# Kernel tuning notes

Hardware: AMD Instinct MI355X
Metric: run time of the kernel (lower is better)

Reference implementation:

```python
import jax, jax.numpy as jnp
import numpy as np

BATCH, FLAT_IN, PROJ_DIM, HEADS, ACT_DIM = 2048, 512, 256, 16384, 64


def setup_inputs() -> dict:
    key = jax.random.key(0)
    k1, k2, k3, k4 = jax.random.split(key, 4)
    state = jax.random.normal(k1, (BATCH, FLAT_IN), dtype=jnp.float32)
    random_projection = jax.random.normal(k2, (FLAT_IN, PROJ_DIM), dtype=jnp.float32)
    memories = jax.random.normal(k3, (HEADS, PROJ_DIM), dtype=jnp.float32)
    logits = jax.random.normal(k4, (HEADS, ACT_DIM), dtype=jnp.float32)
    return {"state": state, "random_projection": random_projection,
            "memories": memories, "logits": logits}


def reference(state, random_projection, memories, logits):
    # state: [B, flat_in] -> projected [B, proj_dim] (proj_dim branch of __call__)
    s = state.reshape(state.shape[0], -1) @ random_projection
    # sum(state[:,None] * memories[None,:], -1) == dot-product similarity GEMM
    similarities = jnp.einsum('bd,hd->bh', s, memories)  # [B, heads]
    closest = jnp.argmax(similarities, axis=1)           # [B]
    return logits[closest]                                # [B, act_dim]
```

## Files before the change

kernel.cpp:

```cpp
#include <hip/hip_runtime.h>

#define BATCH    2048
#define FLAT_IN  512
#define PROJ_DIM 256
#define HEADS    16384
#define ACT_DIM  64

typedef __attribute__((ext_vector_type(8))) short short8;
typedef _Float16 half8 __attribute__((ext_vector_type(8)));
typedef __attribute__((ext_vector_type(4))) float floatx4;

__device__ __forceinline__ unsigned short f2bf(float x) {
  unsigned u = __float_as_uint(x);
  u += 0x7fff + ((u >> 16) & 1);
  return (unsigned short)(u >> 16);
}
__device__ __forceinline__ float bf2f(unsigned short b) {
  return __uint_as_float(((unsigned)b) << 16);
}
__device__ __forceinline__ unsigned short f2h(float x) {
  _Float16 h = (_Float16)x;
  return __builtin_bit_cast(unsigned short, h);
}

#define GLDS16(g, l)                                                          \
  __builtin_amdgcn_global_load_lds(                                           \
      (__attribute__((address_space(1))) void*)(void*)(g),                    \
      (__attribute__((address_space(3))) void*)(l), 16, 0, 0)

__global__ __launch_bounds__(256) void prep(
    const float* __restrict__ state, const float* __restrict__ rp,
    unsigned short* __restrict__ st_hi, unsigned short* __restrict__ st_mid,
    unsigned short* __restrict__ rpT_hi, unsigned short* __restrict__ rpT_mid)
{
  const int tid = threadIdx.x;
  const int b = blockIdx.x;
  if (b < 1024) {
    int i = b * 256 + tid;
    float4 v = ((const float4*)state)[i];
    ushort4 h, m;
    h.x = f2bf(v.x); m.x = f2bf(v.x - bf2f(h.x));
    h.y = f2bf(v.y); m.y = f2bf(v.y - bf2f(h.y));
    h.z = f2bf(v.z); m.z = f2bf(v.z - bf2f(h.z));
    h.w = f2bf(v.w); m.w = f2bf(v.w - bf2f(h.w));
    ((ushort4*)st_hi)[i]  = h;
    ((ushort4*)st_mid)[i] = m;
  } else {
    __shared__ float t[64][65];
    int bid = b - 1024;
    int k0 = (bid >> 2) * 64, n0 = (bid & 3) * 64;
#pragma unroll
    for (int it = 0; it < 16; ++it) {
      int lin = it * 256 + tid;
      int kr = lin >> 6, nc = lin & 63;
      t[kr][nc] = rp[(size_t)(k0 + kr) * PROJ_DIM + n0 + nc];
    }
    __syncthreads();
#pragma unroll
    for (int it = 0; it < 16; ++it) {
      int lin = it * 256 + tid;
      int nr = lin >> 6, kc = lin & 63;
      float v = t[kc][nr];
      unsigned short hh = f2bf(v);
      rpT_hi [(size_t)(n0 + nr) * FLAT_IN + k0 + kc] = hh;
      rpT_mid[(size_t)(n0 + nr) * FLAT_IN + k0 + kc] = f2bf(v - bf2f(hh));
    }
  }
}

__global__ __launch_bounds__(256, 2) void gemm_conv(
    const unsigned short* __restrict__ Ahi, const unsigned short* __restrict__ Amid,
    const unsigned short* __restrict__ Bhi, const unsigned short* __restrict__ Bmid,
    const float* __restrict__ mem,
    float* __restrict__ S, unsigned short* __restrict__ Sf16,
    unsigned short* __restrict__ mem_f16)
{
  const int tid = threadIdx.x;
  if (blockIdx.x >= 128) {
    int i2 = (blockIdx.x - 128) * 256 + tid;
    float4 x = ((const float4*)mem)[2 * i2];
    float4 y = ((const float4*)mem)[2 * i2 + 1];
    short8 o;
    o[0] = (short)f2h(x.x); o[1] = (short)f2h(x.y);
    o[2] = (short)f2h(x.z); o[3] = (short)f2h(x.w);
    o[4] = (short)f2h(y.x); o[5] = (short)f2h(y.y);
    o[6] = (short)f2h(y.z); o[7] = (short)f2h(y.w);
    ((short8*)mem_f16)[i2] = o;
    return;
  }

  __shared__ __align__(16) unsigned short sm[4][64 * 64];
  const int lane = tid & 63, w = tid >> 6;
  const int quad = lane >> 4, col = lane & 15;
  const int wm = (w >> 1) * 32, wn = (w & 1) * 32;
  const int g = blockIdx.x;
  const int m0 = (g & 31) * 64, n0 = (g >> 5) * 64;

  floatx4 acc[2][2];
#pragma unroll
  for (int i = 0; i < 2; ++i)
#pragma unroll
    for (int j = 0; j < 2; ++j) {
      acc[i][j][0] = 0.f; acc[i][j][1] = 0.f;
      acc[i][j][2] = 0.f; acc[i][j][3] = 0.f;
    }

  const int P0 = tid, P1 = tid + 256;
  const int r0 = P0 >> 3, kl0 = (P0 & 7) ^ (r0 & 7);
  const int r1 = P1 >> 3, kl1 = (P1 & 7) ^ (r1 & 7);

  for (int kc = 0; kc < FLAT_IN; kc += 64) {
    GLDS16(Ahi  + (size_t)(m0 + r0) * FLAT_IN + kc + kl0 * 8, &sm[0][P0 * 8]);
    GLDS16(Ahi  + (size_t)(m0 + r1) * FLAT_IN + kc + kl1 * 8, &sm[0][P1 * 8]);
    GLDS16(Amid + (size_t)(m0 + r0) * FLAT_IN + kc + kl0 * 8, &sm[1][P0 * 8]);
    GLDS16(Amid + (size_t)(m0 + r1) * FLAT_IN + kc + kl1 * 8, &sm[1][P1 * 8]);
    GLDS16(Bhi  + (size_t)(n0 + r0) * FLAT_IN + kc + kl0 * 8, &sm[2][P0 * 8]);
    GLDS16(Bhi  + (size_t)(n0 + r1) * FLAT_IN + kc + kl1 * 8, &sm[2][P1 * 8]);
    GLDS16(Bmid + (size_t)(n0 + r0) * FLAT_IN + kc + kl0 * 8, &sm[3][P0 * 8]);
    GLDS16(Bmid + (size_t)(n0 + r1) * FLAT_IN + kc + kl1 * 8, &sm[3][P1 * 8]);
    __syncthreads();

#pragma unroll
    for (int ks = 0; ks < 2; ++ks) {
      short8 bf[2][2];
#pragma unroll
      for (int j = 0; j < 2; ++j) {
        int rr = wn + j * 16 + col;
        int off = rr * 64 + (((ks * 4 + quad) ^ (rr & 7)) * 8);
        bf[j][0] = *(const short8*)&sm[2][off];
        bf[j][1] = *(const short8*)&sm[3][off];
      }
#pragma unroll
      for (int i = 0; i < 2; ++i) {
        int rr = wm + i * 16 + col;
        int off = rr * 64 + (((ks * 4 + quad) ^ (rr & 7)) * 8);
        short8 a0 = *(const short8*)&sm[0][off];
        short8 a1 = *(const short8*)&sm[1][off];
#pragma unroll
        for (int j = 0; j < 2; ++j) {
          acc[i][j] = __builtin_amdgcn_mfma_f32_16x16x32_bf16(a0, bf[j][0], acc[i][j], 0, 0, 0);
          acc[i][j] = __builtin_amdgcn_mfma_f32_16x16x32_bf16(a0, bf[j][1], acc[i][j], 0, 0, 0);
          acc[i][j] = __builtin_amdgcn_mfma_f32_16x16x32_bf16(a1, bf[j][0], acc[i][j], 0, 0, 0);
        }
      }
    }
    __syncthreads();
  }

#pragma unroll
  for (int i = 0; i < 2; ++i)
#pragma unroll
    for (int j = 0; j < 2; ++j)
#pragma unroll
      for (int r = 0; r < 4; ++r) {
        int row = m0 + wm + i * 16 + quad * 4 + r;
        int c   = n0 + wn + j * 16 + col;
        float v = acc[i][j][r];
        S   [(size_t)row * PROJ_DIM + c] = v;
        Sf16[(size_t)row * PROJ_DIM + c] = f2h(v);
      }
}

__global__ __launch_bounds__(512, 4) void sim_topk(
    const unsigned short* __restrict__ Af16,
    const unsigned short* __restrict__ Bf16,
    float2* __restrict__ part2)
{
  __shared__ __align__(16) unsigned short smA[128 * 64];
  __shared__ __align__(16) unsigned short smB[256 * 64];
  const int tid = threadIdx.x;
  const int lane = tid & 63, w = tid >> 6;
  const int quad = lane >> 4, col = lane & 15;
  const int wm = (w >> 2) * 64, wn = (w & 3) * 64;
  const int hc = blockIdx.x;
  const int h0 = hc * 256;
  const int m0 = blockIdx.y * 128;

  floatx4 acc[4][4];
#pragma unroll
  for (int i = 0; i < 4; ++i)
#pragma unroll
    for (int j = 0; j < 4; ++j) {
      acc[i][j][0] = 0.f; acc[i][j][1] = 0.f;
      acc[i][j][2] = 0.f; acc[i][j][3] = 0.f;
    }

  const int PA0 = tid, PA1 = tid + 512;
  const int ra0 = PA0 >> 3, ka0 = (PA0 & 7) ^ (ra0 & 7);
  const int ra1 = PA1 >> 3, ka1 = (PA1 & 7) ^ (ra1 & 7);
  int rb[4], kb[4];
#pragma unroll
  for (int t = 0; t < 4; ++t) {
    int P = t * 512 + tid;
    rb[t] = P >> 3; kb[t] = (P & 7) ^ (rb[t] & 7);
  }

  for (int kc = 0; kc < PROJ_DIM; kc += 64) {
    GLDS16(Af16 + (size_t)(m0 + ra0) * PROJ_DIM + kc + ka0 * 8, &smA[PA0 * 8]);
    GLDS16(Af16 + (size_t)(m0 + ra1) * PROJ_DIM + kc + ka1 * 8, &smA[PA1 * 8]);
#pragma unroll
    for (int t = 0; t < 4; ++t) {
      GLDS16(Bf16 + (size_t)(h0 + rb[t]) * PROJ_DIM + kc + kb[t] * 8,
             &smB[(t * 512 + tid) * 8]);
    }
    __syncthreads();

#pragma unroll
    for (int ks = 0; ks < 2; ++ks) {
      half8 a[4], bfr[4];
#pragma unroll
      for (int i = 0; i < 4; ++i) {
        int rr = wm + i * 16 + col;
        int off = rr * 64 + (((ks * 4 + quad) ^ (rr & 7)) * 8);
        a[i] = *(const half8*)&smA[off];
      }
#pragma unroll
      for (int j = 0; j < 4; ++j) {
        int rr = wn + j * 16 + col;
        int off = rr * 64 + (((ks * 4 + quad) ^ (rr & 7)) * 8);
        bfr[j] = *(const half8*)&smB[off];
      }
#pragma unroll
      for (int i = 0; i < 4; ++i)
#pragma unroll
        for (int j = 0; j < 4; ++j)
          acc[i][j] = __builtin_amdgcn_mfma_f32_16x16x32_f16(a[i], bfr[j], acc[i][j], 0, 0, 0);
    }
    __syncthreads();
  }

#pragma unroll
  for (int i = 0; i < 4; ++i)
#pragma unroll
    for (int r = 0; r < 4; ++r) {
      float b1 = acc[i][0][r]; int h1 = h0 + wn + col;
#pragma unroll
      for (int j = 1; j < 4; ++j) {
        float v = acc[i][j][r]; int h = h0 + wn + j * 16 + col;
        if (v > b1) { b1 = v; h1 = h; }
      }
#pragma unroll
      for (int m = 1; m <= 8; m <<= 1) {
        float ob = __shfl_xor(b1, m); int oh = __shfl_xor(h1, m);
        if (ob > b1 || (ob == b1 && oh < h1)) { b1 = ob; h1 = oh; }
      }
      if (col == 0) {
        int row = m0 + wm + i * 16 + quad * 4 + r;
        part2[((size_t)row * 64 + hc) * 4 + (w & 3)] =
            make_float2(b1, __int_as_float(h1));
      }
    }
}

__global__ __launch_bounds__(64) void finalize(
    const float2* __restrict__ part2, const float* __restrict__ S,
    const float* __restrict__ Mem, const float* __restrict__ logits,
    float* __restrict__ out)
{
  const int row  = blockIdx.x;
  const int lane = threadIdx.x;

  float v[4]; int c[4];
#pragma unroll
  for (int t = 0; t < 4; ++t) {
    float2 p = part2[(size_t)row * 256 + t * 64 + lane];
    v[t] = p.x; c[t] = __float_as_int(p.y);
  }

  int cand[4];
#pragma unroll
  for (int t = 0; t < 4; ++t) {
    float lv = v[0]; int lh = c[0];
#pragma unroll
    for (int q = 1; q < 4; ++q)
      if (v[q] > lv || (v[q] == lv && c[q] < lh)) { lv = v[q]; lh = c[q]; }
#pragma unroll
    for (int d = 32; d; d >>= 1) {
      float ov = __shfl_xor(lv, d); int oh = __shfl_xor(lh, d);
      if (ov > lv || (ov == lv && oh < lh)) { lv = ov; lh = oh; }
    }
    cand[t] = lh;
#pragma unroll
    for (int q = 0; q < 4; ++q)
      if (c[q] == lh) v[q] = -3.4e38f;
  }

  float4 sv = ((const float4*)(S + (size_t)row * PROJ_DIM))[lane];
  float bestv = -3.4e38f; int besth = 0x7fffffff;
#pragma unroll
  for (int t = 0; t < 4; ++t) {
    float4 mv = ((const float4*)(Mem + (size_t)cand[t] * PROJ_DIM))[lane];
    float d = sv.x * mv.x + sv.y * mv.y + sv.z * mv.z + sv.w * mv.w;
#pragma unroll
    for (int s = 32; s; s >>= 1) d += __shfl_xor(d, s);
    if (d > bestv || (d == bestv && cand[t] < besth)) { bestv = d; besth = cand[t]; }
  }
  out[(size_t)row * ACT_DIM + lane] = logits[(size_t)besth * ACT_DIM + lane];
}

extern "C" void kernel_launch(void* const* d_in, const int* in_sizes, int n_in,
                              void* d_out, int out_size, void* d_ws, size_t ws_size,
                              hipStream_t stream) {
  const float* state  = (const float*)d_in[0];
  const float* rp     = (const float*)d_in[1];
  const float* mem    = (const float*)d_in[2];
  const float* logits = (const float*)d_in[3];
  float* out = (float*)d_out;

  char* ws = (char*)d_ws;
  unsigned short* st_hi   = (unsigned short*)(ws);
  unsigned short* st_mid  = (unsigned short*)(ws + (2u  << 20));
  unsigned short* rpT_hi  = (unsigned short*)(ws + (4u  << 20));
  unsigned short* rpT_mid = (unsigned short*)(ws + (4u  << 20) + (256u << 10));
  unsigned short* mem_f16 = (unsigned short*)(ws + (8u  << 20));
  float*          s       = (float*)(ws + (16u << 20));
  unsigned short* s_f16   = (unsigned short*)(ws + (18u << 20));
  float2*         part2   = (float2*)(ws + (20u << 20));

  prep<<<1056, 256, 0, stream>>>(state, rp, st_hi, st_mid, rpT_hi, rpT_mid);

  gemm_conv<<<2176, 256, 0, stream>>>(st_hi, st_mid, rpT_hi, rpT_mid, mem,
                                      s, s_f16, mem_f16);

  sim_topk<<<dim3(64, 16), 512, 0, stream>>>(s_f16, mem_f16, part2);

  finalize<<<BATCH, 64, 0, stream>>>(part2, s, mem, logits, out);
}
```

Measured before the change: 118.4 us.

## Double-buffer sim_topk with larger 256x256 tiles and interleaved MFMA phases

Rewrites the similarity GEMM main loop so each block computes a 256x256 tile, with LDS double-buffered loads of the next K-slice issued between MFMA phases. Explicit vmcnt/lgkmcnt waits, barriers and setprio are used to overlap global-to-LDS traffic with matrix math, and the grid is halved. The finalize kernel also issues all candidate memory-row loads early so they overlap the argmax reduction. In exchange, register and LDS use roughly doubles (128 KB LDS, 128 accumulator floats), which lowers occupancy to two blocks and leaves fewer blocks in the grid.

```diff
diff --git a/kernel.cpp b/kernel.cpp
--- a/kernel.cpp
+++ b/kernel.cpp
@@ -27,6 +27,11 @@
   __builtin_amdgcn_global_load_lds(                                           \
       (__attribute__((address_space(1))) void*)(void*)(g),                    \
       (__attribute__((address_space(3))) void*)(l), 16, 0, 0)
+
+#define BAR()    asm volatile("s_barrier" ::: "memory")
+#define WAITV4() asm volatile("s_waitcnt vmcnt(4)" ::: "memory")
+#define WAITV0() asm volatile("s_waitcnt vmcnt(0)" ::: "memory")
+#define WAITL0() asm volatile("s_waitcnt lgkmcnt(0)" ::: "memory")
 
 __global__ __launch_bounds__(256) void prep(
     const float* __restrict__ state, const float* __restrict__ rp,
@@ -161,82 +166,111 @@
       }
 }
 
-__global__ __launch_bounds__(512, 4) void sim_topk(
+__global__ __launch_bounds__(512, 2) void sim_topk(
     const unsigned short* __restrict__ Af16,
     const unsigned short* __restrict__ Bf16,
     float2* __restrict__ part2)
 {
-  __shared__ __align__(16) unsigned short smA[128 * 64];
-  __shared__ __align__(16) unsigned short smB[256 * 64];
-  const int tid = threadIdx.x;
+  __shared__ __align__(16) unsigned short sm[2][32768];
+  const int tid  = threadIdx.x;
   const int lane = tid & 63, w = tid >> 6;
   const int quad = lane >> 4, col = lane & 15;
-  const int wm = (w >> 2) * 64, wn = (w & 3) * 64;
+  const int wm = (w >> 2) * 128, wn = (w & 3) * 64;
+  const int xb = col & 7;
   const int hc = blockIdx.x;
   const int h0 = hc * 256;
-  const int m0 = blockIdx.y * 128;
-
-  floatx4 acc[4][4];
-#pragma unroll
-  for (int i = 0; i < 4; ++i)
+  const int m0 = blockIdx.y * 256;
+
+  floatx4 acc[8][4];
+#pragma unroll
+  for (int i = 0; i < 8; ++i)
 #pragma unroll
     for (int j = 0; j < 4; ++j) {
       acc[i][j][0] = 0.f; acc[i][j][1] = 0.f;
       acc[i][j][2] = 0.f; acc[i][j][3] = 0.f;
     }
 
-  const int PA0 = tid, PA1 = tid + 512;
-  const int ra0 = PA0 >> 3, ka0 = (PA0 & 7) ^ (ra0 & 7);
-  const int ra1 = PA1 >> 3, ka1 = (PA1 & 7) ^ (ra1 & 7);
-  int rb[4], kb[4];
-#pragma unroll
-  for (int t = 0; t < 4; ++t) {
-    int P = t * 512 + tid;
-    rb[t] = P >> 3; kb[t] = (P & 7) ^ (rb[t] & 7);
-  }
-
-  for (int kc = 0; kc < PROJ_DIM; kc += 64) {
-    GLDS16(Af16 + (size_t)(m0 + ra0) * PROJ_DIM + kc + ka0 * 8, &smA[PA0 * 8]);
-    GLDS16(Af16 + (size_t)(m0 + ra1) * PROJ_DIM + kc + ka1 * 8, &smA[PA1 * 8]);
-#pragma unroll
-    for (int t = 0; t < 4; ++t) {
-      GLDS16(Bf16 + (size_t)(h0 + rb[t]) * PROJ_DIM + kc + kb[t] * 8,
-             &smB[(t * 512 + tid) * 8]);
-    }
-    __syncthreads();
-
-#pragma unroll
-    for (int ks = 0; ks < 2; ++ks) {
-      half8 a[4], bfr[4];
-#pragma unroll
-      for (int i = 0; i < 4; ++i) {
-        int rr = wm + i * 16 + col;
-        int off = rr * 64 + (((ks * 4 + quad) ^ (rr & 7)) * 8);
-        a[i] = *(const half8*)&smA[off];
-      }
-#pragma unroll
-      for (int j = 0; j < 4; ++j) {
-        int rr = wn + j * 16 + col;
-        int off = rr * 64 + (((ks * 4 + quad) ^ (rr & 7)) * 8);
-        bfr[j] = *(const half8*)&smB[off];
-      }
-#pragma unroll
-      for (int i = 0; i < 4; ++i)
-#pragma unroll
-        for (int j = 0; j < 4; ++j)
-          acc[i][j] = __builtin_amdgcn_mfma_f32_16x16x32_f16(a[i], bfr[j], acc[i][j], 0, 0, 0);
-    }
-    __syncthreads();
-  }
-
-#pragma unroll
-  for (int i = 0; i < 4; ++i)
+  const int P0 = tid, P1 = tid + 512;
+  const int r0 = P0 >> 3, c0 = (P0 & 7) ^ (r0 & 7);
+  const int r1 = P1 >> 3, c1 = (P1 & 7) ^ (r1 & 7);
+
+  auto STAGE = [&](int kt, int part) {
+    const unsigned short* src = (part < 2)
+        ? Af16 + (size_t)(m0 + part * 128) * PROJ_DIM
+        : Bf16 + (size_t)(h0 + (part - 2) * 128) * PROJ_DIM;
+    unsigned short* dst = &sm[kt & 1][part * 8192];
+    GLDS16(src + (size_t)r0 * PROJ_DIM + kt * 64 + c0 * 8, dst + P0 * 8);
+    GLDS16(src + (size_t)r1 * PROJ_DIM + kt * 64 + c1 * 8, dst + P1 * 8);
+  };
+
+  auto LDB = [&](half8* b, const unsigned short* Bbuf, int ks) {
+    const int kx = ((ks * 4 + quad) ^ xb) * 8;
+#pragma unroll
+    for (int j = 0; j < 4; ++j) {
+      int rr = wn + j * 16 + col;
+      b[j] = *(const half8*)&Bbuf[rr * 64 + kx];
+    }
+  };
+  auto LDA = [&](half8* a, const unsigned short* Abuf, int mh, int ks) {
+    const int kx = ((ks * 4 + quad) ^ xb) * 8;
+#pragma unroll
+    for (int i = 0; i < 4; ++i) {
+      int rr = wm + mh * 64 + i * 16 + col;
+      a[i] = *(const half8*)&Abuf[rr * 64 + kx];
+    }
+  };
+  auto MM = [&](int IB, half8* a, half8* b) {
+#pragma unroll
+    for (int i = 0; i < 4; ++i)
+#pragma unroll
+      for (int j = 0; j < 4; ++j)
+        acc[IB + i][j] =
+            __builtin_amdgcn_mfma_f32_16x16x32_f16(a[i], b[j], acc[IB + i][j], 0, 0, 0);
+  };
+
+  STAGE(0, 0); STAGE(0, 1); STAGE(0, 2); STAGE(0, 3);
+
+#pragma unroll
+  for (int kt = 0; kt < 4; ++kt) {
+    if (kt < 3) { STAGE(kt + 1, 0); STAGE(kt + 1, 1); WAITV4(); }
+    else        { WAITV0(); }
+    BAR();
+
+    const unsigned short* Abuf = sm[kt & 1];
+    const unsigned short* Bbuf = Abuf + 16384;
+    half8 a[4], b[4];
+
+    LDB(b, Bbuf, 0); LDA(a, Abuf, 0, 0);
+    if (kt < 3) STAGE(kt + 1, 2);
+    BAR(); WAITL0();
+    __builtin_amdgcn_s_setprio(1); MM(0, a, b); __builtin_amdgcn_s_setprio(0);
+    BAR();
+
+    LDA(a, Abuf, 1, 0);
+    if (kt < 3) STAGE(kt + 1, 3);
+    BAR(); WAITL0();
+    __builtin_amdgcn_s_setprio(1); MM(4, a, b); __builtin_amdgcn_s_setprio(0);
+    BAR();
+
+    LDB(b, Bbuf, 1); LDA(a, Abuf, 0, 1);
+    BAR(); WAITL0();
+    __builtin_amdgcn_s_setprio(1); MM(0, a, b); __builtin_amdgcn_s_setprio(0);
+    BAR();
+
+    LDA(a, Abuf, 1, 1);
+    BAR(); WAITL0();
+    __builtin_amdgcn_s_setprio(1); MM(4, a, b); __builtin_amdgcn_s_setprio(0);
+    BAR();
+  }
+
+#pragma unroll
+  for (int I = 0; I < 8; ++I)
 #pragma unroll
     for (int r = 0; r < 4; ++r) {
-      float b1 = acc[i][0][r]; int h1 = h0 + wn + col;
+      float b1 = acc[I][0][r]; int h1 = h0 + wn + col;
 #pragma unroll
       for (int j = 1; j < 4; ++j) {
-        float v = acc[i][j][r]; int h = h0 + wn + j * 16 + col;
+        float v = acc[I][j][r]; int h = h0 + wn + j * 16 + col;
         if (v > b1) { b1 = v; h1 = h; }
       }
 #pragma unroll
@@ -245,7 +279,7 @@
         if (ob > b1 || (ob == b1 && oh < h1)) { b1 = ob; h1 = oh; }
       }
       if (col == 0) {
-        int row = m0 + wm + i * 16 + quad * 4 + r;
+        int row = m0 + wm + (I >> 2) * 64 + (I & 3) * 16 + quad * 4 + r;
         part2[((size_t)row * 64 + hc) * 4 + (w & 3)] =
             make_float2(b1, __int_as_float(h1));
       }
@@ -267,7 +301,7 @@
     v[t] = p.x; c[t] = __float_as_int(p.y);
   }
 
-  int cand[4];
+  int cand[4]; float4 mv[4];
 #pragma unroll
   for (int t = 0; t < 4; ++t) {
     float lv = v[0]; int lh = c[0];
@@ -280,6 +314,7 @@
       if (ov > lv || (ov == lv && oh < lh)) { lv = ov; lh = oh; }
     }
     cand[t] = lh;
+    mv[t] = ((const float4*)(Mem + (size_t)lh * PROJ_DIM))[lane];
 #pragma unroll
     for (int q = 0; q < 4; ++q)
       if (c[q] == lh) v[q] = -3.4e38f;
@@ -289,8 +324,7 @@
   float bestv = -3.4e38f; int besth = 0x7fffffff;
 #pragma unroll
   for (int t = 0; t < 4; ++t) {
-    float4 mv = ((const float4*)(Mem + (size_t)cand[t] * PROJ_DIM))[lane];
-    float d = sv.x * mv.x + sv.y * mv.y + sv.z * mv.z + sv.w * mv.w;
+    float d = sv.x * mv[t].x + sv.y * mv[t].y + sv.z * mv[t].z + sv.w * mv[t].w;
 #pragma unroll
     for (int s = 32; s; s >>= 1) d += __shfl_xor(d, s);
     if (d > bestv || (d == bestv && cand[t] < besth)) { bestv = d; besth = cand[t]; }
@@ -322,7 +356,7 @@
   gemm_conv<<<2176, 256, 0, stream>>>(st_hi, st_mid, rpT_hi, rpT_mid, mem,
                                       s, s_f16, mem_f16);
 
-  sim_topk<<<dim3(64, 16), 512, 0, stream>>>(s_f16, mem_f16, part2);
+  sim_topk<<<dim3(64, 8), 512, 0, stream>>>(s_f16, mem_f16, part2);
 
   finalize<<<BATCH, 64, 0, stream>>>(part2, s, mem, logits, out);
 }
```

New measurement: 129.1 us. 1.09x slower.
